# Kernel optimization log

Measured on AMD Instinct MI355X. Metric: run time of the kernel, lower is better.

The kernel has to match this reference:

```python
import jax, jax.numpy as jnp
import numpy as np

B, S, HID = 2, 1024, 4096
NH, NKV, HD = 32, 8, 128
GROUPS = NH // NKV  # 4
BITS = 8
SCALING = HD ** -0.5


def quantize_lastdim(x, bits=BITS):
    """Asymmetric min-max fake-quant per row of the last dim (groupsize=-1),
    matching ActQuantizer.find_params + quantize/dequantize."""
    qmax = float(2 ** bits - 1)
    xmin = jnp.minimum(jnp.min(x, axis=-1, keepdims=True), 0.0)
    xmax = jnp.maximum(jnp.max(x, axis=-1, keepdims=True), 0.0)
    rng = xmax - xmin
    scale = jnp.where(rng == 0, 1.0, rng / qmax)
    zero = jnp.round(-xmin / scale)
    q = jnp.clip(jnp.round(x / scale) + zero, 0.0, qmax)
    return (q - zero) * scale


def rotate_half(x):
    x1, x2 = jnp.split(x, 2, axis=-1)
    return jnp.concatenate([-x2, x1], axis=-1)


def setup_inputs() -> dict:
    key = jax.random.key(0)
    ks = jax.random.split(key, 5)
    hidden_states = jax.random.normal(ks[0], (B, S, HID), dtype=jnp.float32)
    w_std = 0.02
    Wq = w_std * jax.random.normal(ks[1], (NH * HD, HID), dtype=jnp.float32)
    Wk = w_std * jax.random.normal(ks[2], (NKV * HD, HID), dtype=jnp.float32)
    Wv = w_std * jax.random.normal(ks[3], (NKV * HD, HID), dtype=jnp.float32)
    Wo = w_std * jax.random.normal(ks[4], (HID, NH * HD), dtype=jnp.float32)
    # RoPE tables (theta=10000)
    inv_freq = 1.0 / (10000.0 ** (jnp.arange(0, HD, 2, dtype=jnp.float32) / HD))
    freqs = jnp.outer(jnp.arange(S, dtype=jnp.float32), inv_freq)  # [S, HD/2]
    emb = jnp.concatenate([freqs, freqs], axis=-1)  # [S, HD]
    cos = jnp.broadcast_to(jnp.cos(emb)[None], (B, S, HD)).astype(jnp.float32)
    sin = jnp.broadcast_to(jnp.sin(emb)[None], (B, S, HD)).astype(jnp.float32)
    # additive causal mask [B,1,S,S]
    causal = jnp.tril(jnp.ones((S, S), dtype=bool))
    attention_mask = jnp.where(causal, 0.0, -1e9).astype(jnp.float32)
    attention_mask = jnp.broadcast_to(attention_mask[None, None], (B, 1, S, S))
    return {"hidden_states": hidden_states, "cos": cos, "sin": sin,
            "attention_mask": attention_mask, "Wq": Wq, "Wk": Wk, "Wv": Wv, "Wo": Wo}


def reference(hidden_states, cos, sin, attention_mask, Wq, Wk, Wv, Wo):
    b, s, _ = hidden_states.shape
    # projections -> [B, H, S, D]
    q = (hidden_states @ Wq.T).reshape(b, s, NH, HD).transpose(0, 2, 1, 3)
    k = (hidden_states @ Wk.T).reshape(b, s, NKV, HD).transpose(0, 2, 1, 3)
    v = (hidden_states @ Wv.T).reshape(b, s, NKV, HD).transpose(0, 2, 1, 3)
    # RoPE (HF: unsqueeze cos/sin at head dim)
    c = cos[:, None, :, :]
    si = sin[:, None, :, :]
    q = q * c + rotate_half(q) * si
    k = k * c + rotate_half(k) * si
    # SmoothK per-channel: subtract per-channel mean over the sequence
    # (softmax-invariant outlier smoothing of K before quantization)
    k = k - jnp.mean(k, axis=2, keepdims=True)
    # activation fake-quant of Q, K (per token over head_dim)
    q = quantize_lastdim(q)
    k = quantize_lastdim(k)
    # V quantized along the sequence axis (module transposes dims 2,3 first)
    v = quantize_lastdim(v.transpose(0, 1, 3, 2)).transpose(0, 1, 3, 2)
    # GQA repeat
    k_rep = jnp.repeat(k, GROUPS, axis=1)
    v_rep = jnp.repeat(v, GROUPS, axis=1)
    scores = jnp.einsum('bhqd,bhkd->bhqk', q, k_rep) * SCALING + attention_mask
    w = jax.nn.softmax(scores.astype(jnp.float32), axis=-1).astype(q.dtype)
    # fake-quant attention weights per row (groupsize=-1, so no padding)
    w = quantize_lastdim(w)
    attn = jnp.einsum('bhqk,bhkd->bhqd', w, v_rep)
    attn = attn.transpose(0, 2, 1, 3).reshape(b, s, NH * HD)
    out = attn @ Wo.T
    return (out, w)
```

## Files before the change

kernel.cpp:

```cpp
#include <hip/hip_runtime.h>
#include <math.h>
#include <stdint.h>

typedef unsigned int u32;
typedef unsigned short u16;
typedef __bf16 bf16x8 __attribute__((ext_vector_type(8)));
typedef float f32x4 __attribute__((ext_vector_type(4)));
typedef unsigned short u16x8 __attribute__((ext_vector_type(8)));
typedef unsigned short u16x4 __attribute__((ext_vector_type(4)));

constexpr int   Bb  = 2;
constexpr int   Ss  = 1024;
constexpr int   HID = 4096;
constexpr int   NH  = 32;
constexpr int   NKV = 8;
constexpr int   HD  = 128;
constexpr float SCALING = 0.0883883476483184405501f;

enum { M_QKV = 0, M_OUT = 3 };

__device__ __forceinline__ u16 f2bf(float f) {
  u32 u = __builtin_bit_cast(u32, f);
  u = u + 0x7fffu + ((u >> 16) & 1u);
  return (u16)(u >> 16);
}

__device__ __forceinline__ void gld_lds16(const void* g, void* l) {
  __builtin_amdgcn_global_load_lds(
      (const __attribute__((address_space(1))) u32*)(uintptr_t)g,
      (__attribute__((address_space(3))) u32*)(uintptr_t)l, 16, 0, 0);
}

template <int MODE>
__global__ __launch_bounds__(256, 3) void mfma_gemm(
    const u16* __restrict__ Abf_g,
    const u16* __restrict__ B0, const u16* __restrict__ B1,
    const u16* __restrict__ B2,
    float* __restrict__ Cf, float* __restrict__ Ck, float* __restrict__ Cv,
    int K) {
  __shared__ u16 As[3][128 * 32];
  __shared__ u16 Bs[3][128 * 32];

  const int tid = threadIdx.x;
  const int lane = tid & 63;
  const int wid = tid >> 6;
  const int wr = wid >> 1, wc = wid & 1;

  const int m0 = blockIdx.y * 128;
  int nloc = blockIdx.x * 128;

  const u16* Abf = Abf_g + (size_t)m0 * K;
  const u16* Bp = nullptr;
  int which = 0;

  if (MODE == M_QKV) {
    const int j = blockIdx.x;
    if (j < 32)      { which = 0; Bp = B0 + (size_t)j * 128 * K;        nloc = j * 128; }
    else if (j < 40) { which = 1; Bp = B1 + (size_t)(j - 32) * 128 * K; nloc = (j - 32) * 128; }
    else             { which = 2; Bp = B2 + (size_t)(j - 40) * 128 * K; nloc = (j - 40) * 128; }
  } else {
    Bp = B0 + (size_t)nloc * K;
  }

  f32x4 acc[4][4];
#pragma unroll
  for (int i = 0; i < 4; i++)
#pragma unroll
    for (int j = 0; j < 4; j++) acc[i][j] = (f32x4){0.f, 0.f, 0.f, 0.f};

  const int sr = lane >> 2;
  const int sp = lane & 3;
  const int fr = lane & 15;
  const int fq = lane >> 4;

  const int nk = K >> 5;

#pragma unroll
  for (int p = 0; p < 2; ++p) {
#pragma unroll
    for (int cc = 0; cc < 2; ++cc) {
      const int c = wid + cc * 4;
      const int r = c * 16 + sr;
      const int go = (sp ^ ((r >> 1) & 3)) * 8;
      gld_lds16(Abf + (size_t)r * K + p * 32 + go, &As[p][c * 512]);
      gld_lds16(Bp + (size_t)r * K + p * 32 + go, &Bs[p][c * 512]);
    }
  }
  asm volatile("s_waitcnt vmcnt(4)" ::: "memory");
  __builtin_amdgcn_sched_barrier(0);
  __builtin_amdgcn_s_barrier();

  int cur = 0;
  for (int kt = 0; kt < nk; ++kt) {
    if (kt + 2 < nk) {
      const int stg = (cur == 0) ? 2 : cur - 1;
#pragma unroll
      for (int cc = 0; cc < 2; ++cc) {
        const int c = wid + cc * 4;
        const int r = c * 16 + sr;
        const int go = (sp ^ ((r >> 1) & 3)) * 8;
        gld_lds16(Abf + (size_t)r * K + (kt + 2) * 32 + go, &As[stg][c * 512]);
        gld_lds16(Bp + (size_t)r * K + (kt + 2) * 32 + go, &Bs[stg][c * 512]);
      }
    }

    bf16x8 av[4], bv[4];
#pragma unroll
    for (int f = 0; f < 4; ++f) {
      const int ra = wr * 64 + f * 16 + fr;
      av[f] = *(const bf16x8*)&As[cur][ra * 32 + ((fq ^ ((ra >> 1) & 3)) * 8)];
      const int rb = wc * 64 + f * 16 + fr;
      bv[f] = *(const bf16x8*)&Bs[cur][rb * 32 + ((fq ^ ((rb >> 1) & 3)) * 8)];
    }

    __builtin_amdgcn_s_setprio(1);
#pragma unroll
    for (int i = 0; i < 4; i++)
#pragma unroll
      for (int j = 0; j < 4; j++)
        acc[i][j] = __builtin_amdgcn_mfma_f32_16x16x32_bf16(av[i], bv[j], acc[i][j], 0, 0, 0);
    __builtin_amdgcn_s_setprio(0);

    if (kt + 2 < nk) {
      asm volatile("s_waitcnt vmcnt(4)" ::: "memory");
    } else {
      asm volatile("s_waitcnt vmcnt(0)" ::: "memory");
    }
    __builtin_amdgcn_sched_barrier(0);
    __builtin_amdgcn_s_barrier();
    cur = (cur == 2) ? 0 : cur + 1;
  }

#pragma unroll
  for (int i = 0; i < 4; i++) {
#pragma unroll
    for (int j = 0; j < 4; j++) {
      const int n = nloc + wc * 64 + j * 16 + fr;
#pragma unroll
      for (int e = 0; e < 4; e++) {
        const int m = m0 + wr * 64 + i * 16 + fq * 4 + e;
        float val = acc[i][j][e];
        if (MODE == M_QKV) {
          const int b = m >> 10, s = m & 1023, h = n >> 7, d = n & 127;
          if (which == 0)      Cf[((size_t)(b * NH + h) * Ss + s) * HD + d] = val;
          else if (which == 1) Ck[((size_t)(b * NKV + h) * Ss + s) * HD + d] = val;
          else                 Cv[((size_t)(b * NKV + h) * HD + d) * Ss + s] = val;
        } else {
          Cf[(size_t)m * HID + n] = val;
        }
      }
    }
  }
}

__global__ __launch_bounds__(256) void fused_attn(
    const u16* __restrict__ qb,
    const u16* __restrict__ kb,
    const u16* __restrict__ vTb,
    float* __restrict__ wout,
    u16* __restrict__ attnb) {
  __shared__ u16 Ks[64 * 128];
  __shared__ u16 Vs[128 * 64];
  __shared__ u16 plds[4][16 * 64];
  __shared__ float scl_l[4][16];

  const int a = 15 - (int)(blockIdx.x >> 6);
  const int bh = blockIdx.x & 63;
  const int b = bh >> 5, h = bh & 31;
  const int kv = h >> 2;
  const int tid = threadIdx.x;
  const int lane = tid & 63;
  const int wq = tid >> 6;
  const int fr = lane & 15, fq = lane >> 4;

  const int nt = a + 1;
  const int Q0 = a * 64;
  const int qw0 = Q0 + wq * 16;

  const u16* Kb = kb + (size_t)(b * NKV + kv) * Ss * HD;
  const u16* Vb = vTb + (size_t)(b * NKV + kv) * HD * Ss;
  float* wrow = wout + (size_t)bh * Ss * Ss;

  if (a < 15) {
    const int base = 64 * nt;
    const int n4 = 16 * (15 - a);
#pragma unroll
    for (int r0 = 0; r0 < 4; ++r0) {
      const int row = Q0 + r0 * 16 + (tid >> 4);
      float4* wp = (float4*)&wrow[(size_t)row * Ss + base];
      for (int c = tid & 15; c < n4; c += 16) wp[c] = float4{0.f, 0.f, 0.f, 0.f};
    }
  }

  bf16x8 qf[4];
#pragma unroll
  for (int kk = 0; kk < 4; kk++)
    qf[kk] = *(const bf16x8*)&qb[((size_t)bh * Ss + qw0 + fr) * HD + kk * 32 + fq * 8];

  float m[4], l[4];
#pragma unroll
  for (int i = 0; i < 4; i++) { m[i] = -1e30f; l[i] = 0.f; }

  for (int t = 0; t < nt; ++t) {
    __syncthreads();
#pragma unroll
    for (int c = 0; c < 4; ++c) {
      const int idx0 = (c * 4 + wq) * 64;
      const int idx = idx0 + lane;
      const int row = idx >> 4, sl = idx & 15;
      const int slot = sl ^ (row & 15);
      gld_lds16(Kb + (size_t)(t * 64 + row) * HD + slot * 8, &Ks[idx0 * 8]);
    }
    __syncthreads();

    f32x4 sa[4];
#pragma unroll
    for (int jn = 0; jn < 4; jn++) sa[jn] = (f32x4){0.f, 0.f, 0.f, 0.f};
#pragma unroll
    for (int kk = 0; kk < 4; ++kk) {
      bf16x8 kfv[4];
#pragma unroll
      for (int jn = 0; jn < 4; ++jn) {
        const int row = jn * 16 + fr;
        kfv[jn] = *(const bf16x8*)&Ks[row * 128 + (((kk * 4 + fq) ^ fr) * 8)];
      }
#pragma unroll
      for (int jn = 0; jn < 4; ++jn)
        sa[jn] = __builtin_amdgcn_mfma_f32_16x16x32_bf16(qf[kk], kfv[jn], sa[jn], 0, 0, 0);
    }

    const bool diag = (t == a);
#pragma unroll
    for (int e = 0; e < 4; ++e) {
      const int qrow = qw0 + fq * 4 + e;
      float sv[4];
      float rmax = -1e30f;
#pragma unroll
      for (int jn = 0; jn < 4; ++jn) {
        float s = sa[jn][e] * SCALING;
        if (diag && (t * 64 + jn * 16 + fr > qrow)) s = -1e30f;
        sv[jn] = s;
        rmax = fmaxf(rmax, s);
      }
#pragma unroll
      for (int o = 1; o < 16; o <<= 1) rmax = fmaxf(rmax, __shfl_xor(rmax, o));
      const float mn = fmaxf(m[e], rmax);
      const float cc = __expf(m[e] - mn);
      float rs = __expf(sv[0] - mn) + __expf(sv[1] - mn) +
                 __expf(sv[2] - mn) + __expf(sv[3] - mn);
#pragma unroll
      for (int o = 1; o < 16; o <<= 1) rs += __shfl_xor(rs, o);
      l[e] = l[e] * cc + rs;
      m[e] = mn;
    }
  }

  float scl[4];
#pragma unroll
  for (int e = 0; e < 4; e++) scl[e] = 1.f / (255.f * l[e]);
  if (fr == 0) {
#pragma unroll
    for (int e = 0; e < 4; e++) scl_l[wq][fq * 4 + e] = scl[e];
  }

  f32x4 acc2[8];
#pragma unroll
  for (int j = 0; j < 8; j++) acc2[j] = (f32x4){0.f, 0.f, 0.f, 0.f};

  u16* pl = &plds[wq][0];
  const int wrrow = lane >> 2, wrq = lane & 3;
  const float sclr = scl_l[wq][wrrow];

  for (int t = 0; t < nt; ++t) {
    __syncthreads();
#pragma unroll
    for (int c = 0; c < 4; ++c) {
      const int idx0 = (c * 4 + wq) * 64;
      const int idx = idx0 + lane;
      {
        const int row = idx >> 4, sl = idx & 15;
        const int slot = sl ^ (row & 15);
        gld_lds16(Kb + (size_t)(t * 64 + row) * HD + slot * 8, &Ks[idx0 * 8]);
      }
      {
        const int d = idx >> 3, sl = idx & 7;
        const int slot = sl ^ (d & 7);
        gld_lds16(Vb + (size_t)d * Ss + t * 64 + slot * 8, &Vs[idx0 * 8]);
      }
    }
    __syncthreads();

    f32x4 sa[4];
#pragma unroll
    for (int jn = 0; jn < 4; jn++) sa[jn] = (f32x4){0.f, 0.f, 0.f, 0.f};
#pragma unroll
    for (int kk = 0; kk < 4; ++kk) {
      bf16x8 kfv[4];
#pragma unroll
      for (int jn = 0; jn < 4; ++jn) {
        const int row = jn * 16 + fr;
        kfv[jn] = *(const bf16x8*)&Ks[row * 128 + (((kk * 4 + fq) ^ fr) * 8)];
      }
#pragma unroll
      for (int jn = 0; jn < 4; ++jn)
        sa[jn] = __builtin_amdgcn_mfma_f32_16x16x32_bf16(qf[kk], kfv[jn], sa[jn], 0, 0, 0);
    }

    const bool diag = (t == a);
#pragma unroll
    for (int e = 0; e < 4; ++e) {
      const int qrow = qw0 + fq * 4 + e;
      const int r16 = fq * 4 + e;
#pragma unroll
      for (int jn = 0; jn < 4; ++jn) {
        const int kc = t * 64 + jn * 16 + fr;
        float qv = 0.f;
        if (!diag || kc <= qrow)
          qv = rintf(fminf(255.f * __expf(sa[jn][e] * SCALING - m[e]), 255.f));
        const int col = jn * 16 + fr;
        const int byte = r16 * 128 + (((col >> 3) ^ (r16 & 7)) * 16) + (col & 7) * 2;
        *(u16*)((char*)pl + byte) = f2bf(qv);
      }
    }

    {
      const int s0 = (2 * wrq) ^ (wrrow & 7);
      const int s1 = (2 * wrq + 1) ^ (wrrow & 7);
      bf16x8 p0 = *(const bf16x8*)((char*)pl + wrrow * 128 + s0 * 16);
      bf16x8 p1 = *(const bf16x8*)((char*)pl + wrrow * 128 + s1 * 16);
      float* wp = &wrow[(size_t)(qw0 + wrrow) * Ss + t * 64 + wrq * 16];
      float4 o0, o1, o2, o3;
      o0.x = (float)p0[0] * sclr; o0.y = (float)p0[1] * sclr;
      o0.z = (float)p0[2] * sclr; o0.w = (float)p0[3] * sclr;
      o1.x = (float)p0[4] * sclr; o1.y = (float)p0[5] * sclr;
      o1.z = (float)p0[6] * sclr; o1.w = (float)p0[7] * sclr;
      o2.x = (float)p1[0] * sclr; o2.y = (float)p1[1] * sclr;
      o2.z = (float)p1[2] * sclr; o2.w = (float)p1[3] * sclr;
      o3.x = (float)p1[4] * sclr; o3.y = (float)p1[5] * sclr;
      o3.z = (float)p1[6] * sclr; o3.w = (float)p1[7] * sclr;
      ((float4*)wp)[0] = o0; ((float4*)wp)[1] = o1;
      ((float4*)wp)[2] = o2; ((float4*)wp)[3] = o3;
    }

#pragma unroll
    for (int kk2 = 0; kk2 < 2; ++kk2) {
      const bf16x8 pa = *(const bf16x8*)((char*)pl + fr * 128 + (((kk2 * 4 + fq) ^ (fr & 7)) * 16));
#pragma unroll
      for (int jn2 = 0; jn2 < 8; ++jn2) {
        const int d = jn2 * 16 + fr;
        const bf16x8 vb = *(const bf16x8*)&Vs[d * 64 + (((kk2 * 4 + fq) ^ (d & 7)) * 8)];
        acc2[jn2] = __builtin_amdgcn_mfma_f32_16x16x32_bf16(pa, vb, acc2[jn2], 0, 0, 0);
      }
    }
  }

#pragma unroll
  for (int e = 0; e < 4; ++e) {
    const int qrow = qw0 + fq * 4 + e;
#pragma unroll
    for (int jn2 = 0; jn2 < 8; ++jn2)
      attnb[((size_t)b * Ss + qrow) * HID + h * HD + jn2 * 16 + fr] =
          f2bf(acc2[jn2][e] * scl[e]);
  }
}

__global__ __launch_bounds__(256) void f32_to_bf16_k(const float* __restrict__ in,
                                                     u16* __restrict__ out, int n8) {
  const int i = blockIdx.x * 256 + threadIdx.x;
  if (i < n8) {
    float4 a = ((const float4*)in)[2 * i];
    float4 b = ((const float4*)in)[2 * i + 1];
    u16x8 t;
    t[0] = f2bf(a.x); t[1] = f2bf(a.y); t[2] = f2bf(a.z); t[3] = f2bf(a.w);
    t[4] = f2bf(b.x); t[5] = f2bf(b.y); t[6] = f2bf(b.z); t[7] = f2bf(b.w);
    ((u16x8*)out)[i] = t;
  }
}

__global__ __launch_bounds__(256) void rope_quant_q(const float* __restrict__ q,
                                                    u16* __restrict__ qb,
                                                    const float* __restrict__ cs,
                                                    const float* __restrict__ sn) {
  const int row = blockIdx.x * 4 + (threadIdx.x >> 6);
  const int lane = threadIdx.x & 63;
  const int s = row & (Ss - 1);
  const int b = row >> 15;
  const float* p = q + (size_t)row * HD;
  const float* cp = cs + ((size_t)b * Ss + s) * HD;
  const float* sp = sn + ((size_t)b * Ss + s) * HD;
  float x1 = p[lane], x2 = p[lane + 64];
  float r1 = x1 * cp[lane] - x2 * sp[lane];
  float r2 = x2 * cp[lane + 64] + x1 * sp[lane + 64];
  float mn = fminf(0.f, fminf(r1, r2));
  float mx = fmaxf(0.f, fmaxf(r1, r2));
#pragma unroll
  for (int o = 32; o; o >>= 1) {
    mn = fminf(mn, __shfl_xor(mn, o));
    mx = fmaxf(mx, __shfl_xor(mx, o));
  }
  float rng = mx - mn;
  float scale = (rng == 0.f) ? 1.f : rng / 255.f;
  float zero = rintf(-mn / scale);
  float q1 = fminf(fmaxf(rintf(r1 / scale) + zero, 0.f), 255.f);
  float q2 = fminf(fmaxf(rintf(r2 / scale) + zero, 0.f), 255.f);
  qb[(size_t)row * HD + lane] = f2bf((q1 - zero) * scale);
  qb[(size_t)row * HD + lane + 64] = f2bf((q2 - zero) * scale);
}

__global__ __launch_bounds__(256) void rope_k(float* __restrict__ k,
                                              const float* __restrict__ cs,
                                              const float* __restrict__ sn) {
  const int row = blockIdx.x * 4 + (threadIdx.x >> 6);
  const int lane = threadIdx.x & 63;
  const int s = row & (Ss - 1);
  const int b = row >> 13;
  float* p = k + (size_t)row * HD;
  const float* cp = cs + ((size_t)b * Ss + s) * HD;
  const float* sp = sn + ((size_t)b * Ss + s) * HD;
  float x1 = p[lane], x2 = p[lane + 64];
  float r1 = x1 * cp[lane] - x2 * sp[lane];
  float r2 = x2 * cp[lane + 64] + x1 * sp[lane + 64];
  p[lane] = r1;
  p[lane + 64] = r2;
}

__global__ __launch_bounds__(1024) void kmean_kernel(const float* __restrict__ k,
                                                     float* __restrict__ kmean) {
  const int bh = blockIdx.x;
  const int d = threadIdx.x & 127;
  const int sl = threadIdx.x >> 7;
  const float* p = k + (size_t)bh * Ss * HD;
  float sum = 0.f;
  for (int s = sl; s < Ss; s += 8) sum += p[(size_t)s * HD + d];
  __shared__ float lds[8][128];
  lds[sl][d] = sum;
  __syncthreads();
  if (threadIdx.x < 128) {
    float t = 0.f;
#pragma unroll
    for (int i = 0; i < 8; i++) t += lds[i][threadIdx.x];
    kmean[bh * HD + threadIdx.x] = t * (1.f / 1024.f);
  }
}

__global__ __launch_bounds__(256) void k_subquant(const float* __restrict__ k,
                                                  u16* __restrict__ kb,
                                                  const float* __restrict__ kmean) {
  const int row = blockIdx.x * 4 + (threadIdx.x >> 6);
  const int lane = threadIdx.x & 63;
  const int bh = row >> 10;
  const float* p = k + (size_t)row * HD;
  float x1 = p[lane] - kmean[bh * HD + lane];
  float x2 = p[lane + 64] - kmean[bh * HD + lane + 64];
  float mn = fminf(0.f, fminf(x1, x2));
  float mx = fmaxf(0.f, fmaxf(x1, x2));
#pragma unroll
  for (int o = 32; o; o >>= 1) {
    mn = fminf(mn, __shfl_xor(mn, o));
    mx = fmaxf(mx, __shfl_xor(mx, o));
  }
  float rng = mx - mn;
  float scale = (rng == 0.f) ? 1.f : rng / 255.f;
  float zero = rintf(-mn / scale);
  float q1 = fminf(fmaxf(rintf(x1 / scale) + zero, 0.f), 255.f);
  float q2 = fminf(fmaxf(rintf(x2 / scale) + zero, 0.f), 255.f);
  kb[(size_t)row * HD + lane] = f2bf((q1 - zero) * scale);
  kb[(size_t)row * HD + lane + 64] = f2bf((q2 - zero) * scale);
}

__global__ __launch_bounds__(256) void vquant(const float* __restrict__ vT,
                                              u16* __restrict__ vTb) {
  const float* p = vT + (size_t)blockIdx.x * Ss;
  const int t = threadIdx.x;
  float4 x = ((const float4*)p)[t];
  float mn = fminf(0.f, fminf(fminf(x.x, x.y), fminf(x.z, x.w)));
  float mx = fmaxf(0.f, fmaxf(fmaxf(x.x, x.y), fmaxf(x.z, x.w)));
#pragma unroll
  for (int o = 32; o; o >>= 1) {
    mn = fminf(mn, __shfl_xor(mn, o));
    mx = fmaxf(mx, __shfl_xor(mx, o));
  }
  __shared__ float smn[4], smx[4];
  const int wid = t >> 6, lane = t & 63;
  if (lane == 0) { smn[wid] = mn; smx[wid] = mx; }
  __syncthreads();
  mn = fminf(fminf(smn[0], smn[1]), fminf(smn[2], smn[3]));
  mx = fmaxf(fmaxf(smx[0], smx[1]), fmaxf(smx[2], smx[3]));
  float rng = mx - mn;
  float scale = (rng == 0.f) ? 1.f : rng / 255.f;
  float zero = rintf(-mn / scale);
  u16x4 o4;
  o4[0] = f2bf((fminf(fmaxf(rintf(x.x / scale) + zero, 0.f), 255.f) - zero) * scale);
  o4[1] = f2bf((fminf(fmaxf(rintf(x.y / scale) + zero, 0.f), 255.f) - zero) * scale);
  o4[2] = f2bf((fminf(fmaxf(rintf(x.z / scale) + zero, 0.f), 255.f) - zero) * scale);
  o4[3] = f2bf((fminf(fmaxf(rintf(x.w / scale) + zero, 0.f), 255.f) - zero) * scale);
  ((u16x4*)vTb)[(size_t)blockIdx.x * 256 + t] = o4;
}

extern "C" void kernel_launch(void* const* d_in, const int* in_sizes, int n_in,
                              void* d_out, int out_size, void* d_ws, size_t ws_size,
                              hipStream_t stream) {
  const float* hs = (const float*)d_in[0];
  const float* cosp = (const float*)d_in[1];
  const float* sinp = (const float*)d_in[2];
  const float* Wq = (const float*)d_in[4];
  const float* Wk = (const float*)d_in[5];
  const float* Wv = (const float*)d_in[6];
  const float* Wo = (const float*)d_in[7];

  float* out = (float*)d_out;
  float* wout = out + (size_t)Bb * Ss * HID;

  char* wsp = (char*)d_ws;
  auto alloc = [&](size_t bytes) {
    char* p = wsp;
    wsp += (bytes + 255) & ~(size_t)255;
    return p;
  };
  float* q     = (float*)alloc((size_t)Bb * NH * Ss * HD * 4);
  float* k     = (float*)alloc((size_t)Bb * NKV * Ss * HD * 4);
  float* vT    = (float*)alloc((size_t)Bb * NKV * Ss * HD * 4);
  float* kmean = (float*)alloc((size_t)Bb * NKV * HD * 4);
  u16* hsb = (u16*)alloc((size_t)Bb * Ss * HID * 2);
  u16* qb  = (u16*)alloc((size_t)Bb * NH * Ss * HD * 2);
  u16* kb  = (u16*)alloc((size_t)Bb * NKV * Ss * HD * 2);
  u16* vTb = (u16*)alloc((size_t)Bb * NKV * Ss * HD * 2);
  u16* Wqb = (u16*)alloc((size_t)NH * HD * HID * 2);
  u16* Wkb = (u16*)alloc((size_t)NKV * HD * HID * 2);
  u16* Wvb = (u16*)alloc((size_t)NKV * HD * HID * 2);
  u16* Wob = (u16*)alloc((size_t)HID * NH * HD * 2);
  u16* attnb = (u16*)q;

  f32_to_bf16_k<<<(Bb * Ss * HID / 8 + 255) / 256, 256, 0, stream>>>(hs, hsb, Bb * Ss * HID / 8);
  f32_to_bf16_k<<<(NH * HD * HID / 8 + 255) / 256, 256, 0, stream>>>(Wq, Wqb, NH * HD * HID / 8);
  f32_to_bf16_k<<<(NKV * HD * HID / 8 + 255) / 256, 256, 0, stream>>>(Wk, Wkb, NKV * HD * HID / 8);
  f32_to_bf16_k<<<(NKV * HD * HID / 8 + 255) / 256, 256, 0, stream>>>(Wv, Wvb, NKV * HD * HID / 8);
  f32_to_bf16_k<<<(HID * NH * HD / 8 + 255) / 256, 256, 0, stream>>>(Wo, Wob, HID * NH * HD / 8);

  mfma_gemm<M_QKV><<<dim3(48, 16, 1), 256, 0, stream>>>(
      hsb, Wqb, Wkb, Wvb, q, k, vT, HID);

  rope_quant_q<<<(Bb * NH * Ss) / 4, 256, 0, stream>>>(q, qb, cosp, sinp);
  rope_k<<<(Bb * NKV * Ss) / 4, 256, 0, stream>>>(k, cosp, sinp);
  kmean_kernel<<<Bb * NKV, 1024, 0, stream>>>(k, kmean);
  k_subquant<<<(Bb * NKV * Ss) / 4, 256, 0, stream>>>(k, kb, kmean);
  vquant<<<Bb * NKV * HD, 256, 0, stream>>>(vT, vTb);

  fused_attn<<<dim3(1024), 256, 0, stream>>>(qb, kb, vTb, wout, attnb);

  mfma_gemm<M_OUT><<<dim3(32, 16, 1), 256, 0, stream>>>(
      attnb, Wob, nullptr, nullptr, out, nullptr, nullptr, HID);
}
```

Baseline: 453.9 us.

## Enlarge GEMM tiles to 256-row blocks with 4-stage pipeline and merge conversion kernels

```diff
diff --git a/kernel.cpp b/kernel.cpp
--- a/kernel.cpp
+++ b/kernel.cpp
@@ -31,23 +31,26 @@
       (__attribute__((address_space(3))) u32*)(uintptr_t)l, 16, 0, 0);
 }
 
-template <int MODE>
-__global__ __launch_bounds__(256, 3) void mfma_gemm(
+template <int MODE, int NREP>
+__global__ __launch_bounds__(512) void mfma_gemm(
     const u16* __restrict__ Abf_g,
     const u16* __restrict__ B0, const u16* __restrict__ B1,
     const u16* __restrict__ B2,
     float* __restrict__ Cf, float* __restrict__ Ck, float* __restrict__ Cv,
     int K) {
-  __shared__ u16 As[3][128 * 32];
-  __shared__ u16 Bs[3][128 * 32];
+  constexpr int BN = NREP * 64;
+  constexpr int BCW = BN / 128;
+  __shared__ u16 As[4][256 * 32];
+  __shared__ u16 Bs[4][BN * 32];
 
   const int tid = threadIdx.x;
   const int lane = tid & 63;
   const int wid = tid >> 6;
-  const int wr = wid >> 1, wc = wid & 1;
-
-  const int m0 = blockIdx.y * 128;
-  int nloc = blockIdx.x * 128;
+  const int wr = wid >> 2;
+  const int wc = wid & 3;
+
+  const int m0 = blockIdx.y * 256;
+  int nloc = 0;
 
   const u16* Abf = Abf_g + (size_t)m0 * K;
   const u16* Bp = nullptr;
@@ -55,90 +58,98 @@
 
   if (MODE == M_QKV) {
     const int j = blockIdx.x;
-    if (j < 32)      { which = 0; Bp = B0 + (size_t)j * 128 * K;        nloc = j * 128; }
-    else if (j < 40) { which = 1; Bp = B1 + (size_t)(j - 32) * 128 * K; nloc = (j - 32) * 128; }
-    else             { which = 2; Bp = B2 + (size_t)(j - 40) * 128 * K; nloc = (j - 40) * 128; }
+    if (j < 16)      { which = 0; Bp = B0 + (size_t)j * 256 * K;        nloc = j * 256; }
+    else if (j < 20) { which = 1; Bp = B1 + (size_t)(j - 16) * 256 * K; nloc = (j - 16) * 256; }
+    else             { which = 2; Bp = B2 + (size_t)(j - 20) * 256 * K; nloc = (j - 20) * 256; }
   } else {
-    Bp = B0 + (size_t)nloc * K;
-  }
-
-  f32x4 acc[4][4];
-#pragma unroll
-  for (int i = 0; i < 4; i++)
-#pragma unroll
-    for (int j = 0; j < 4; j++) acc[i][j] = (f32x4){0.f, 0.f, 0.f, 0.f};
-
-  const int sr = lane >> 2;
-  const int sp = lane & 3;
+    Bp = B0 + (size_t)blockIdx.x * BN * K;
+    nloc = blockIdx.x * BN;
+  }
+
+  f32x4 acc[8][NREP];
+#pragma unroll
+  for (int i = 0; i < 8; i++)
+#pragma unroll
+    for (int j = 0; j < NREP; j++) acc[i][j] = (f32x4){0.f, 0.f, 0.f, 0.f};
+
   const int fr = lane & 15;
   const int fq = lane >> 4;
+  const int srow = lane >> 2;
+  const int ssl = lane & 3;
 
   const int nk = K >> 5;
 
-#pragma unroll
-  for (int p = 0; p < 2; ++p) {
+  auto stage = [&](int t, int sbuf) {
+    const int ko = t * 32;
 #pragma unroll
     for (int cc = 0; cc < 2; ++cc) {
-      const int c = wid + cc * 4;
-      const int r = c * 16 + sr;
-      const int go = (sp ^ ((r >> 1) & 3)) * 8;
-      gld_lds16(Abf + (size_t)r * K + p * 32 + go, &As[p][c * 512]);
-      gld_lds16(Bp + (size_t)r * K + p * 32 + go, &Bs[p][c * 512]);
-    }
-  }
-  asm volatile("s_waitcnt vmcnt(4)" ::: "memory");
+      const int c = wid * 2 + cc;
+      const int r = c * 16 + srow;
+      gld_lds16(Abf + (size_t)r * K + ko + ((ssl ^ ((r >> 1) & 3)) * 8),
+                &As[sbuf][c * 512]);
+    }
+#pragma unroll
+    for (int cc = 0; cc < BCW; ++cc) {
+      const int c = wid * BCW + cc;
+      const int r = c * 16 + srow;
+      gld_lds16(Bp + (size_t)r * K + ko + ((ssl ^ ((r >> 1) & 3)) * 8),
+                &Bs[sbuf][c * 512]);
+    }
+  };
+
+  stage(0, 0);
+  stage(1, 1);
+  stage(2, 2);
+  if (NREP == 4) { asm volatile("s_waitcnt vmcnt(8)" ::: "memory"); }
+  else           { asm volatile("s_waitcnt vmcnt(6)" ::: "memory"); }
   __builtin_amdgcn_sched_barrier(0);
   __builtin_amdgcn_s_barrier();
 
-  int cur = 0;
   for (int kt = 0; kt < nk; ++kt) {
-    if (kt + 2 < nk) {
-      const int stg = (cur == 0) ? 2 : cur - 1;
-#pragma unroll
-      for (int cc = 0; cc < 2; ++cc) {
-        const int c = wid + cc * 4;
-        const int r = c * 16 + sr;
-        const int go = (sp ^ ((r >> 1) & 3)) * 8;
-        gld_lds16(Abf + (size_t)r * K + (kt + 2) * 32 + go, &As[stg][c * 512]);
-        gld_lds16(Bp + (size_t)r * K + (kt + 2) * 32 + go, &Bs[stg][c * 512]);
-      }
-    }
-
-    bf16x8 av[4], bv[4];
-#pragma unroll
-    for (int f = 0; f < 4; ++f) {
-      const int ra = wr * 64 + f * 16 + fr;
-      av[f] = *(const bf16x8*)&As[cur][ra * 32 + ((fq ^ ((ra >> 1) & 3)) * 8)];
-      const int rb = wc * 64 + f * 16 + fr;
-      bv[f] = *(const bf16x8*)&Bs[cur][rb * 32 + ((fq ^ ((rb >> 1) & 3)) * 8)];
+    const int cur = kt & 3;
+    if (kt + 3 < nk) stage(kt + 3, (kt + 3) & 3);
+
+    bf16x8 av[8], bv[NREP];
+#pragma unroll
+    for (int i = 0; i < 8; ++i) {
+      const int r = wr * 128 + i * 16 + fr;
+      av[i] = *(const bf16x8*)&As[cur][r * 32 + ((fq ^ ((r >> 1) & 3)) * 8)];
+    }
+#pragma unroll
+    for (int j = 0; j < NREP; ++j) {
+      const int r = wc * (NREP * 16) + j * 16 + fr;
+      bv[j] = *(const bf16x8*)&Bs[cur][r * 32 + ((fq ^ ((r >> 1) & 3)) * 8)];
     }
 
     __builtin_amdgcn_s_setprio(1);
 #pragma unroll
-    for (int i = 0; i < 4; i++)
-#pragma unroll
-      for (int j = 0; j < 4; j++)
+    for (int i = 0; i < 8; i++)
+#pragma unroll
+      for (int j = 0; j < NREP; j++)
         acc[i][j] = __builtin_amdgcn_mfma_f32_16x16x32_bf16(av[i], bv[j], acc[i][j], 0, 0, 0);
     __builtin_amdgcn_s_setprio(0);
 
-    if (kt + 2 < nk) {
-      asm volatile("s_waitcnt vmcnt(4)" ::: "memory");
+    if (kt + 3 < nk) {
+      if (NREP == 4) { asm volatile("s_waitcnt vmcnt(8)" ::: "memory"); }
+      else           { asm volatile("s_waitcnt vmcnt(6)" ::: "memory"); }
+    } else if (kt + 3 == nk) {
+      if (NREP == 4) { asm volatile("s_waitcnt vmcnt(4)" ::: "memory"); }
+      else           { asm volatile("s_waitcnt vmcnt(3)" ::: "memory"); }
     } else {
       asm volatile("s_waitcnt vmcnt(0)" ::: "memory");
     }
     __builtin_amdgcn_sched_barrier(0);
     __builtin_amdgcn_s_barrier();
-    cur = (cur == 2) ? 0 : cur + 1;
-  }
-
-#pragma unroll
-  for (int i = 0; i < 4; i++) {
-#pragma unroll
-    for (int j = 0; j < 4; j++) {
-      const int n = nloc + wc * 64 + j * 16 + fr;
+  }
+
+#pragma unroll
+  for (int i = 0; i < 8; i++) {
+#pragma unroll
+    for (int j = 0; j < NREP; j++) {
+      const int n = nloc + wc * (NREP * 16) + j * 16 + fr;
 #pragma unroll
       for (int e = 0; e < 4; e++) {
-        const int m = m0 + wr * 64 + i * 16 + fq * 4 + e;
+        const int m = m0 + wr * 128 + i * 16 + fq * 4 + e;
         float val = acc[i][j][e];
         if (MODE == M_QKV) {
           const int b = m >> 10, s = m & 1023, h = n >> 7, d = n & 127;
@@ -364,17 +375,34 @@
   }
 }
 
-__global__ __launch_bounds__(256) void f32_to_bf16_k(const float* __restrict__ in,
-                                                     u16* __restrict__ out, int n8) {
-  const int i = blockIdx.x * 256 + threadIdx.x;
-  if (i < n8) {
-    float4 a = ((const float4*)in)[2 * i];
-    float4 b = ((const float4*)in)[2 * i + 1];
-    u16x8 t;
-    t[0] = f2bf(a.x); t[1] = f2bf(a.y); t[2] = f2bf(a.z); t[3] = f2bf(a.w);
-    t[4] = f2bf(b.x); t[5] = f2bf(b.y); t[6] = f2bf(b.z); t[7] = f2bf(b.w);
-    ((u16x8*)out)[i] = t;
-  }
+constexpr int CB_HS = Bb * Ss * HID / 2048;
+constexpr int CB_WQ = NH * HD * HID / 2048;
+constexpr int CB_WK = NKV * HD * HID / 2048;
+constexpr int CB_WV = CB_WK;
+constexpr int CB_WO = HID * NH * HD / 2048;
+
+__global__ __launch_bounds__(256) void convert_all(
+    const float* __restrict__ hs, const float* __restrict__ wq,
+    const float* __restrict__ wk, const float* __restrict__ wv,
+    const float* __restrict__ wo,
+    u16* __restrict__ hsb, u16* __restrict__ wqb, u16* __restrict__ wkb,
+    u16* __restrict__ wvb, u16* __restrict__ wob) {
+  const int bid = blockIdx.x;
+  const float* src;
+  u16* dst;
+  int base;
+  if (bid < CB_HS) { src = hs; dst = hsb; base = 0; }
+  else if (bid < CB_HS + CB_WQ) { src = wq; dst = wqb; base = CB_HS; }
+  else if (bid < CB_HS + CB_WQ + CB_WK) { src = wk; dst = wkb; base = CB_HS + CB_WQ; }
+  else if (bid < CB_HS + CB_WQ + CB_WK + CB_WV) { src = wv; dst = wvb; base = CB_HS + CB_WQ + CB_WK; }
+  else { src = wo; dst = wob; base = CB_HS + CB_WQ + CB_WK + CB_WV; }
+  const int i = (bid - base) * 256 + threadIdx.x;
+  float4 a = ((const float4*)src)[2 * i];
+  float4 b = ((const float4*)src)[2 * i + 1];
+  u16x8 t;
+  t[0] = f2bf(a.x); t[1] = f2bf(a.y); t[2] = f2bf(a.z); t[3] = f2bf(a.w);
+  t[4] = f2bf(b.x); t[5] = f2bf(b.y); t[6] = f2bf(b.z); t[7] = f2bf(b.w);
+  ((u16x8*)dst)[i] = t;
 }
 
 __global__ __launch_bounds__(256) void rope_quant_q(const float* __restrict__ q,
@@ -531,13 +559,10 @@
   u16* Wob = (u16*)alloc((size_t)HID * NH * HD * 2);
   u16* attnb = (u16*)q;
 
-  f32_to_bf16_k<<<(Bb * Ss * HID / 8 + 255) / 256, 256, 0, stream>>>(hs, hsb, Bb * Ss * HID / 8);
-  f32_to_bf16_k<<<(NH * HD * HID / 8 + 255) / 256, 256, 0, stream>>>(Wq, Wqb, NH * HD * HID / 8);
-  f32_to_bf16_k<<<(NKV * HD * HID / 8 + 255) / 256, 256, 0, stream>>>(Wk, Wkb, NKV * HD * HID / 8);
-  f32_to_bf16_k<<<(NKV * HD * HID / 8 + 255) / 256, 256, 0, stream>>>(Wv, Wvb, NKV * HD * HID / 8);
-  f32_to_bf16_k<<<(HID * NH * HD / 8 + 255) / 256, 256, 0, stream>>>(Wo, Wob, HID * NH * HD / 8);
-
-  mfma_gemm<M_QKV><<<dim3(48, 16, 1), 256, 0, stream>>>(
+  convert_all<<<CB_HS + CB_WQ + CB_WK + CB_WV + CB_WO, 256, 0, stream>>>(
+      hs, Wq, Wk, Wv, Wo, hsb, Wqb, Wkb, Wvb, Wob);
+
+  mfma_gemm<M_QKV, 4><<<dim3(24, 8), 512, 0, stream>>>(
       hsb, Wqb, Wkb, Wvb, q, k, vT, HID);
 
   rope_quant_q<<<(Bb * NH * Ss) / 4, 256, 0, stream>>>(q, qb, cosp, sinp);
@@ -548,6 +573,6 @@
 
   fused_attn<<<dim3(1024), 256, 0, stream>>>(qb, kb, vTb, wout, attnb);
 
-  mfma_gemm<M_OUT><<<dim3(32, 16, 1), 256, 0, stream>>>(
+  mfma_gemm<M_OUT, 2><<<dim3(32, 8), 512, 0, stream>>>(
       attnb, Wob, nullptr, nullptr, out, nullptr, nullptr, HID);
 }
```

New measurement: 446.6 us. Within noise of the previous version (-1.6%).
